# Kernel optimization log

Measured on AMD Instinct MI355X. Metric: run time of the kernel, lower is better.

## Reference

```python
import math
import jax, jax.numpy as jnp
import numpy as np

PHI = (1.0 + math.sqrt(5.0)) / 2.0
LUT_N = 4096
TWO_PI = 2.0 * math.pi


def _lut_tables():
    angles = jnp.arange(LUT_N, dtype=jnp.float32) * (TWO_PI / LUT_N)
    return jnp.sin(angles), jnp.cos(angles)


def _lut_sin_cos(theta, sin_t, cos_t):
    # quantize angle to nearest LUT entry, wrap mod 2*pi
    idx = jnp.mod(jnp.round(theta * (LUT_N / TWO_PI)).astype(jnp.int32), LUT_N)
    return jnp.take(sin_t, idx), jnp.take(cos_t, idx)


def setup_inputs() -> dict:
    key = jax.random.key(0)
    ks = jax.random.split(key, 8)
    B, D, H = 4096, 4096, 16
    Dh = D // H
    return {
        'x_real': jax.random.normal(ks[0], (B, D), dtype=jnp.float32),
        'x_imag': jax.random.normal(ks[1], (B, D), dtype=jnp.float32),
        't': jax.random.uniform(ks[2], (B,), dtype=jnp.float32) * 100.0,
        'trigger_real': jax.random.normal(ks[3], (H, Dh), dtype=jnp.float32) * 0.5,
        'trigger_imag': jax.random.normal(ks[4], (H, Dh), dtype=jnp.float32) * 0.5,
        'w_query': jax.random.normal(ks[5], (H, Dh), dtype=jnp.float32) * 0.02,
        'b_query': jnp.zeros((H, Dh), dtype=jnp.float32),
        'w_out': jax.random.normal(ks[6], (D,), dtype=jnp.float32) * 0.02,
        'b_out': jnp.zeros((D,), dtype=jnp.float32),
        'beta': jnp.abs(jax.random.normal(ks[7], (D,), dtype=jnp.float32)) * 5.0 + 5.0,
    }


def reference(x_real, x_imag, t, trigger_real, trigger_imag, w_query, b_query, w_out, b_out, beta):
    sin_t, cos_t = _lut_tables()
    B, D = x_real.shape
    H, Dh = trigger_real.shape

    # ---- per-head interference (vectorized over heads) ----
    xr = x_real.reshape(B, H, Dh)
    xi = x_imag.reshape(B, H, Dh)
    t_phi_h = (t * PHI)[:, None, None]                       # (B,1,1)
    wavelength_q = 1.0 + jnp.abs(w_query)                    # (H,Dh)
    theta_r = xr / wavelength_q + b_query + t_phi_h
    theta_i = xi / wavelength_q + b_query + t_phi_h
    sin_r, cos_r = _lut_sin_cos(theta_r, sin_t, cos_t)
    sin_i, cos_i = _lut_sin_cos(theta_i, sin_t, cos_t)
    q_real = cos_r * cos_i - sin_r * sin_i                   # (B,H,Dh)
    q_imag = cos_r * sin_i + sin_r * cos_i
    int_r = (q_real * trigger_real + q_imag * trigger_imag).sum(-1)   # (B,H)
    int_i = (q_real * trigger_imag - q_imag * trigger_real).sum(-1)
    total_int_real = int_r.mean(-1)                          # (B,)
    total_int_imag = int_i.mean(-1)

    # ---- constant-Q memory update (fresh memory = zeros) ----
    beta_eff = 1.0 / (1.0 + jnp.abs(beta))                   # (D,)
    w_eff = 1.0 / (1.0 + jnp.abs(w_out))                     # (D,)
    decay = jnp.minimum(jnp.exp(-beta_eff * w_eff), 0.9999)
    int_mag = jnp.sqrt(total_int_real ** 2 + total_int_imag ** 2 + 1e-8)[:, None]  # (B,1)
    write_scale = (w_eff * (1.0 - decay))[None, :]           # (1,D)
    # initial memory is zero -> memory*decay term vanishes
    mem_real = x_real * int_mag * write_scale
    mem_imag = x_imag * int_mag * write_scale

    # ---- Euler projection of memory ----
    wavelength = 1.0 + jnp.abs(w_out)
    t_phi = (t * PHI)[:, None]
    th_or = mem_real / wavelength + b_out + t_phi
    th_oi = mem_imag / wavelength + b_out + t_phi
    sin_or, cos_or = _lut_sin_cos(th_or, sin_t, cos_t)
    sin_oi, cos_oi = _lut_sin_cos(th_oi, sin_t, cos_t)
    out_real = cos_or * cos_oi - sin_or * sin_oi
    out_imag = cos_or * sin_oi + sin_or * cos_oi
    return out_real, out_imag
```

## Files before the change

### kernel.cpp

```cpp
#include <hip/hip_runtime.h>

#define LUT_N 4096
#define DVAL  4096
#define TPB   256

static constexpr double TWO_PI_D = 6.283185307179586476925286766559;
#define PHI_F 1.61803398874989484820f

__device__ __forceinline__ float fc(const float4& f, int j) {
    switch (j) { case 0: return f.x; case 1: return f.y; case 2: return f.z; }
    return f.w;
}
__device__ __forceinline__ void sc4(float4& f, int j, float v) {
    switch (j) { case 0: f.x = v; return; case 1: f.y = v; return; case 2: f.z = v; return; }
    f.w = v;
}
__device__ __forceinline__ void grid_sincos(float thr, float thi, float cidx,
                                            float& s_out, float& c_out) {
    float r = rintf(thr * cidx);
    float s = rintf(thi * cidx);
    float rev = (r + s) * (1.0f / (float)LUT_N);
    float frac = rev - floorf(rev);
    s_out = __builtin_amdgcn_sinf(frac);
    c_out = __builtin_amdgcn_cosf(frac);
}

__global__ __launch_bounds__(256) void echo_precompute(
    const float* __restrict__ w_query,
    const float* __restrict__ w_out,
    const float* __restrict__ beta,
    float* __restrict__ invq,
    float* __restrict__ wsi)
{
    int i = blockIdx.x * 256 + threadIdx.x;
    if (i < DVAL) {
        float inv_q     = 1.0f / (1.0f + fabsf(w_query[i]));
        float w_eff     = 1.0f / (1.0f + fabsf(w_out[i]));
        float beta_eff  = 1.0f / (1.0f + fabsf(beta[i]));
        float decay     = fminf(expf(-beta_eff * w_eff), 0.9999f);
        invq[i] = inv_q;
        wsi[i]  = (w_eff * (1.0f - decay)) * w_eff;
    }
}

template<bool USE_WS>
__global__ __launch_bounds__(TPB, 4) void echo_main(
    const float* __restrict__ x_real,
    const float* __restrict__ x_imag,
    const float* __restrict__ t,
    const float* __restrict__ trig_r,
    const float* __restrict__ trig_i,
    const float* __restrict__ w_query,
    const float* __restrict__ b_query,
    const float* __restrict__ w_out,
    const float* __restrict__ b_out,
    const float* __restrict__ beta,
    const float* __restrict__ invqG,
    const float* __restrict__ wsiG,
    float* __restrict__ out,
    int B)
{
    __shared__ float redR[4], redI[4];
    __shared__ float magS;

    const int tid = threadIdx.x;
    const int row = blockIdx.x;
    const float cidx = (float)((double)LUT_N / TWO_PI_D);

    const float tphi = t[row] * PHI_F;
    const float* xr = x_real + (size_t)row * DVAL;
    const float* xi = x_imag + (size_t)row * DVAL;

    float4 xr_s[4], xi_s[4];
    float accr = 0.0f, acci = 0.0f;

    #pragma unroll
    for (int k = 0; k < 4; ++k) {
        int v = tid + TPB * k;
        float4 a = ((const float4*)xr)[v];
        float4 c = ((const float4*)xi)[v];
        xr_s[k] = a; xi_s[k] = c;

        float4 iv4;
        if constexpr (USE_WS) {
            iv4 = ((const float4*)invqG)[v];
        } else {
            float4 wq4 = ((const float4*)w_query)[v];
            iv4 = make_float4(1.0f / (1.0f + fabsf(wq4.x)), 1.0f / (1.0f + fabsf(wq4.y)),
                              1.0f / (1.0f + fabsf(wq4.z)), 1.0f / (1.0f + fabsf(wq4.w)));
        }
        float4 bq4 = ((const float4*)b_query)[v];
        float4 tr4 = ((const float4*)trig_r)[v];
        float4 ti4 = ((const float4*)trig_i)[v];

        #pragma unroll
        for (int j = 0; j < 4; ++j) {
            float iv = fc(iv4, j), bq = fc(bq4, j);
            float thr = __builtin_fmaf(fc(a, j), iv, bq) + tphi;
            float thi = __builtin_fmaf(fc(c, j), iv, bq) + tphi;
            float q_i, q_r;
            grid_sincos(thr, thi, cidx, q_i, q_r);
            accr = __builtin_fmaf(q_r, fc(tr4, j), __builtin_fmaf(q_i, fc(ti4, j), accr));
            acci = __builtin_fmaf(q_r, fc(ti4, j), __builtin_fmaf(-q_i, fc(tr4, j), acci));
        }
    }

    #pragma unroll
    for (int m = 32; m >= 1; m >>= 1) {
        accr += __shfl_xor(accr, m, 64);
        acci += __shfl_xor(acci, m, 64);
    }
    if ((tid & 63) == 0) { redR[tid >> 6] = accr; redI[tid >> 6] = acci; }
    __syncthreads();
    if (tid == 0) {
        float tr = (redR[0] + redR[1] + redR[2] + redR[3]) * 0.0625f;
        float ti = (redI[0] + redI[1] + redI[2] + redI[3]) * 0.0625f;
        magS = sqrtf(tr * tr + ti * ti + 1e-8f);
    }
    __syncthreads();
    const float mag = magS;

    float4* outR = (float4*)(out + (size_t)row * DVAL);
    float4* outI = (float4*)(out + (size_t)B * DVAL + (size_t)row * DVAL);

    #pragma unroll
    for (int k = 0; k < 4; ++k) {
        int v = tid + TPB * k;
        float4 ws4;
        if constexpr (USE_WS) {
            ws4 = ((const float4*)wsiG)[v];
        } else {
            float4 wo4 = ((const float4*)w_out)[v];
            float4 be4 = ((const float4*)beta)[v];
            #pragma unroll
            for (int j = 0; j < 4; ++j) {
                float w_eff = 1.0f / (1.0f + fabsf(fc(wo4, j)));
                float beta_eff = 1.0f / (1.0f + fabsf(fc(be4, j)));
                float decay = fminf(expf(-beta_eff * w_eff), 0.9999f);
                sc4(ws4, j, (w_eff * (1.0f - decay)) * w_eff);
            }
        }
        float4 bo4 = ((const float4*)b_out)[v];

        float4 oR, oI;
        #pragma unroll
        for (int j = 0; j < 4; ++j) {
            float wsi_j = fc(ws4, j), bo = fc(bo4, j);
            float xmr = fc(xr_s[k], j) * mag;
            float xmi = fc(xi_s[k], j) * mag;
            float thr = __builtin_fmaf(xmr, wsi_j, bo) + tphi;
            float thi = __builtin_fmaf(xmi, wsi_j, bo) + tphi;
            float s_o, c_o;
            grid_sincos(thr, thi, cidx, s_o, c_o);
            sc4(oR, j, c_o);
            sc4(oI, j, s_o);
        }
        outR[v] = oR;
        outI[v] = oI;
    }
}

extern "C" void kernel_launch(void* const* d_in, const int* in_sizes, int n_in,
                              void* d_out, int out_size, void* d_ws, size_t ws_size,
                              hipStream_t stream) {
    const float* x_real    = (const float*)d_in[0];
    const float* x_imag    = (const float*)d_in[1];
    const float* t         = (const float*)d_in[2];
    const float* trig_r    = (const float*)d_in[3];
    const float* trig_i    = (const float*)d_in[4];
    const float* w_query   = (const float*)d_in[5];
    const float* b_query   = (const float*)d_in[6];
    const float* w_out     = (const float*)d_in[7];
    const float* b_out     = (const float*)d_in[8];
    const float* beta      = (const float*)d_in[9];
    float* out = (float*)d_out;

    const int B = in_sizes[2];
    const size_t need = 2 * (size_t)DVAL * sizeof(float);

    if (d_ws != nullptr && ws_size >= need) {
        float* invq = (float*)d_ws;
        float* wsi  = invq + DVAL;
        echo_precompute<<<DVAL / 256, 256, 0, stream>>>(w_query, w_out, beta, invq, wsi);
        echo_main<true><<<B, TPB, 0, stream>>>(
            x_real, x_imag, t, trig_r, trig_i, w_query, b_query, w_out, b_out, beta,
            invq, wsi, out, B);
    } else {
        echo_main<false><<<B, TPB, 0, stream>>>(
            x_real, x_imag, t, trig_r, trig_i, w_query, b_query, w_out, b_out, beta,
            nullptr, nullptr, out, B);
    }
}
```

Baseline: 261.8 us.

## Split fused row kernel into magnitude reduction and grid-stride projection kernels

Replaces the single per-row kernel with two launches: one computes the per-row interference magnitude into workspace, and a second grid-stride kernel does the Euler projection over all elements. This removes the in-block barrier between reduction and projection and decouples their occupancy. In exchange, x_real and x_imag are read from memory twice, and the workspace must now also hold B floats.

```diff
diff --git a/kernel.cpp b/kernel.cpp
--- a/kernel.cpp
+++ b/kernel.cpp
@@ -43,8 +43,117 @@
     }
 }
 
-template<bool USE_WS>
-__global__ __launch_bounds__(TPB, 4) void echo_main(
+__global__ __launch_bounds__(TPB) void echo_mag(
+    const float* __restrict__ x_real,
+    const float* __restrict__ x_imag,
+    const float* __restrict__ t,
+    const float* __restrict__ trig_r,
+    const float* __restrict__ trig_i,
+    const float* __restrict__ b_query,
+    const float* __restrict__ invqG,
+    float* __restrict__ magG)
+{
+    __shared__ float redR[4], redI[4];
+
+    const int tid = threadIdx.x;
+    const int row = blockIdx.x;
+    const float cidx = (float)((double)LUT_N / TWO_PI_D);
+
+    const float tphi = t[row] * PHI_F;
+    const float* xr = x_real + (size_t)row * DVAL;
+    const float* xi = x_imag + (size_t)row * DVAL;
+
+    float accr = 0.0f, acci = 0.0f;
+
+    #pragma unroll
+    for (int k = 0; k < 4; ++k) {
+        int v = tid + TPB * k;
+        float4 a   = ((const float4*)xr)[v];
+        float4 c   = ((const float4*)xi)[v];
+        float4 iv4 = ((const float4*)invqG)[v];
+        float4 bq4 = ((const float4*)b_query)[v];
+        float4 tr4 = ((const float4*)trig_r)[v];
+        float4 ti4 = ((const float4*)trig_i)[v];
+
+        #pragma unroll
+        for (int j = 0; j < 4; ++j) {
+            float iv = fc(iv4, j), bq = fc(bq4, j);
+            float thr = __builtin_fmaf(fc(a, j), iv, bq) + tphi;
+            float thi = __builtin_fmaf(fc(c, j), iv, bq) + tphi;
+            float q_i, q_r;
+            grid_sincos(thr, thi, cidx, q_i, q_r);
+            accr = __builtin_fmaf(q_r, fc(tr4, j), __builtin_fmaf(q_i, fc(ti4, j), accr));
+            acci = __builtin_fmaf(q_r, fc(ti4, j), __builtin_fmaf(-q_i, fc(tr4, j), acci));
+        }
+    }
+
+    #pragma unroll
+    for (int m = 32; m >= 1; m >>= 1) {
+        accr += __shfl_xor(accr, m, 64);
+        acci += __shfl_xor(acci, m, 64);
+    }
+    if ((tid & 63) == 0) { redR[tid >> 6] = accr; redI[tid >> 6] = acci; }
+    __syncthreads();
+    if (tid == 0) {
+        float tr = (redR[0] + redR[1] + redR[2] + redR[3]) * 0.0625f;
+        float ti = (redI[0] + redI[1] + redI[2] + redI[3]) * 0.0625f;
+        magG[row] = sqrtf(tr * tr + ti * ti + 1e-8f);
+    }
+}
+
+__global__ __launch_bounds__(TPB, 4) void echo_proj(
+    const float* __restrict__ x_real,
+    const float* __restrict__ x_imag,
+    const float* __restrict__ t,
+    const float* __restrict__ b_out,
+    const float* __restrict__ wsiG,
+    const float* __restrict__ magG,
+    float* __restrict__ out,
+    int B, int nblocks)
+{
+    const float cidx = (float)((double)LUT_N / TWO_PI_D);
+    const int nvec_row = DVAL / 4;
+    const long total   = (long)B * nvec_row;
+    const long stride  = (long)nblocks * TPB;
+    long g = (long)blockIdx.x * TPB + threadIdx.x;
+
+    const float4* xr4 = (const float4*)x_real;
+    const float4* xi4 = (const float4*)x_imag;
+    const float4* bo4G = (const float4*)b_out;
+    const float4* ws4G = (const float4*)wsiG;
+    float4* outR = (float4*)out;
+    float4* outI = (float4*)(out + (size_t)B * DVAL);
+
+    #pragma unroll 4
+    for (long i = g; i < total; i += stride) {
+        int row  = (int)(i >> 10);
+        int col4 = (int)(i & 1023);
+
+        float4 a   = xr4[i];
+        float4 c   = xi4[i];
+        float4 ws4 = ws4G[col4];
+        float4 bo  = bo4G[col4];
+        float mag  = magG[row];
+        float tphi = t[row] * PHI_F;
+
+        float4 oR, oI;
+        #pragma unroll
+        for (int j = 0; j < 4; ++j) {
+            float xmr = fc(a, j) * mag;
+            float xmi = fc(c, j) * mag;
+            float thr = __builtin_fmaf(xmr, fc(ws4, j), fc(bo, j)) + tphi;
+            float thi = __builtin_fmaf(xmi, fc(ws4, j), fc(bo, j)) + tphi;
+            float s_o, c_o;
+            grid_sincos(thr, thi, cidx, s_o, c_o);
+            sc4(oR, j, c_o);
+            sc4(oI, j, s_o);
+        }
+        outR[i] = oR;
+        outI[i] = oI;
+    }
+}
+
+__global__ __launch_bounds__(TPB, 4) void echo_single(
     const float* __restrict__ x_real,
     const float* __restrict__ x_imag,
     const float* __restrict__ t,
@@ -55,8 +164,6 @@
     const float* __restrict__ w_out,
     const float* __restrict__ b_out,
     const float* __restrict__ beta,
-    const float* __restrict__ invqG,
-    const float* __restrict__ wsiG,
     float* __restrict__ out,
     int B)
 {
@@ -80,19 +187,12 @@
         float4 a = ((const float4*)xr)[v];
         float4 c = ((const float4*)xi)[v];
         xr_s[k] = a; xi_s[k] = c;
-
-        float4 iv4;
-        if constexpr (USE_WS) {
-            iv4 = ((const float4*)invqG)[v];
-        } else {
-            float4 wq4 = ((const float4*)w_query)[v];
-            iv4 = make_float4(1.0f / (1.0f + fabsf(wq4.x)), 1.0f / (1.0f + fabsf(wq4.y)),
-                              1.0f / (1.0f + fabsf(wq4.z)), 1.0f / (1.0f + fabsf(wq4.w)));
-        }
+        float4 wq4 = ((const float4*)w_query)[v];
+        float4 iv4 = make_float4(1.0f / (1.0f + fabsf(wq4.x)), 1.0f / (1.0f + fabsf(wq4.y)),
+                                 1.0f / (1.0f + fabsf(wq4.z)), 1.0f / (1.0f + fabsf(wq4.w)));
         float4 bq4 = ((const float4*)b_query)[v];
         float4 tr4 = ((const float4*)trig_r)[v];
         float4 ti4 = ((const float4*)trig_i)[v];
-
         #pragma unroll
         for (int j = 0; j < 4; ++j) {
             float iv = fc(iv4, j), bq = fc(bq4, j);
@@ -104,7 +204,6 @@
             acci = __builtin_fmaf(q_r, fc(ti4, j), __builtin_fmaf(-q_i, fc(tr4, j), acci));
         }
     }
-
     #pragma unroll
     for (int m = 32; m >= 1; m >>= 1) {
         accr += __shfl_xor(accr, m, 64);
@@ -122,34 +221,27 @@
 
     float4* outR = (float4*)(out + (size_t)row * DVAL);
     float4* outI = (float4*)(out + (size_t)B * DVAL + (size_t)row * DVAL);
-
     #pragma unroll
     for (int k = 0; k < 4; ++k) {
         int v = tid + TPB * k;
+        float4 wo4 = ((const float4*)w_out)[v];
+        float4 be4 = ((const float4*)beta)[v];
         float4 ws4;
-        if constexpr (USE_WS) {
-            ws4 = ((const float4*)wsiG)[v];
-        } else {
-            float4 wo4 = ((const float4*)w_out)[v];
-            float4 be4 = ((const float4*)beta)[v];
-            #pragma unroll
-            for (int j = 0; j < 4; ++j) {
-                float w_eff = 1.0f / (1.0f + fabsf(fc(wo4, j)));
-                float beta_eff = 1.0f / (1.0f + fabsf(fc(be4, j)));
-                float decay = fminf(expf(-beta_eff * w_eff), 0.9999f);
-                sc4(ws4, j, (w_eff * (1.0f - decay)) * w_eff);
-            }
+        #pragma unroll
+        for (int j = 0; j < 4; ++j) {
+            float w_eff = 1.0f / (1.0f + fabsf(fc(wo4, j)));
+            float beta_eff = 1.0f / (1.0f + fabsf(fc(be4, j)));
+            float decay = fminf(expf(-beta_eff * w_eff), 0.9999f);
+            sc4(ws4, j, (w_eff * (1.0f - decay)) * w_eff);
         }
         float4 bo4 = ((const float4*)b_out)[v];
-
         float4 oR, oI;
         #pragma unroll
         for (int j = 0; j < 4; ++j) {
-            float wsi_j = fc(ws4, j), bo = fc(bo4, j);
             float xmr = fc(xr_s[k], j) * mag;
             float xmi = fc(xi_s[k], j) * mag;
-            float thr = __builtin_fmaf(xmr, wsi_j, bo) + tphi;
-            float thi = __builtin_fmaf(xmi, wsi_j, bo) + tphi;
+            float thr = __builtin_fmaf(xmr, fc(ws4, j), fc(bo4, j)) + tphi;
+            float thi = __builtin_fmaf(xmi, fc(ws4, j), fc(bo4, j)) + tphi;
             float s_o, c_o;
             grid_sincos(thr, thi, cidx, s_o, c_o);
             sc4(oR, j, c_o);
@@ -176,18 +268,21 @@
     float* out = (float*)d_out;
 
     const int B = in_sizes[2];
-    const size_t need = 2 * (size_t)DVAL * sizeof(float);
+    const size_t need = (2 * (size_t)DVAL + (size_t)B) * sizeof(float);
 
     if (d_ws != nullptr && ws_size >= need) {
         float* invq = (float*)d_ws;
         float* wsi  = invq + DVAL;
+        float* mag  = wsi + DVAL;
         echo_precompute<<<DVAL / 256, 256, 0, stream>>>(w_query, w_out, beta, invq, wsi);
-        echo_main<true><<<B, TPB, 0, stream>>>(
+        echo_mag<<<B, TPB, 0, stream>>>(x_real, x_imag, t, trig_r, trig_i, b_query,
+                                        invq, mag);
+        const int nblocks = 2048;
+        echo_proj<<<nblocks, TPB, 0, stream>>>(x_real, x_imag, t, b_out, wsi, mag,
+                                               out, B, nblocks);
+    } else {
+        echo_single<<<B, TPB, 0, stream>>>(
             x_real, x_imag, t, trig_r, trig_i, w_query, b_query, w_out, b_out, beta,
-            invq, wsi, out, B);
-    } else {
-        echo_main<false><<<B, TPB, 0, stream>>>(
-            x_real, x_imag, t, trig_r, trig_i, w_query, b_query, w_out, b_out, beta,
-            nullptr, nullptr, out, B);
-    }
-}
+            out, B);
+    }
+}
```

After: 276.7 us. 5.7% more time.

## Process four rows per block with register double-buffered prefetch of next row

Applied to the files above, without the earlier changes.

Each block now handles four consecutive rows instead of one. While it computes the current row, it loads the next row's x_real/x_imag into a second set of registers, so global memory latency overlaps with compute. This cuts the grid size by four and doubles the registers used for row data, which can lower occupancy under the launch bounds and reduce the number of blocks available to balance across CUs. Rows beyond B are clamped to B-1, which recomputes and rewrites the last row.

```diff
diff --git a/kernel.cpp b/kernel.cpp
--- a/kernel.cpp
+++ b/kernel.cpp
@@ -3,6 +3,7 @@
 #define LUT_N 4096
 #define DVAL  4096
 #define TPB   256
+#define RPB   4
 
 static constexpr double TWO_PI_D = 6.283185307179586476925286766559;
 #define PHI_F 1.61803398874989484820f
@@ -44,7 +45,7 @@
 }
 
 template<bool USE_WS>
-__global__ __launch_bounds__(TPB, 4) void echo_main(
+__global__ __launch_bounds__(TPB, 4) void echo_persist(
     const float* __restrict__ x_real,
     const float* __restrict__ x_imag,
     const float* __restrict__ t,
@@ -63,100 +64,128 @@
     __shared__ float redR[4], redI[4];
     __shared__ float magS;
 
-    const int tid = threadIdx.x;
-    const int row = blockIdx.x;
+    const int tid  = threadIdx.x;
+    const int row0 = blockIdx.x * RPB;
     const float cidx = (float)((double)LUT_N / TWO_PI_D);
 
-    const float tphi = t[row] * PHI_F;
-    const float* xr = x_real + (size_t)row * DVAL;
-    const float* xi = x_imag + (size_t)row * DVAL;
-
-    float4 xr_s[4], xi_s[4];
-    float accr = 0.0f, acci = 0.0f;
+    float4 curR[4], curI[4], nxtR[4], nxtI[4];
+
+    {
+        int row = min(row0, B - 1);
+        const float4* xr4 = (const float4*)(x_real + (size_t)row * DVAL);
+        const float4* xi4 = (const float4*)(x_imag + (size_t)row * DVAL);
+        #pragma unroll
+        for (int k = 0; k < 4; ++k) {
+            curR[k] = xr4[tid + TPB * k];
+            curI[k] = xi4[tid + TPB * k];
+        }
+    }
 
     #pragma unroll
-    for (int k = 0; k < 4; ++k) {
-        int v = tid + TPB * k;
-        float4 a = ((const float4*)xr)[v];
-        float4 c = ((const float4*)xi)[v];
-        xr_s[k] = a; xi_s[k] = c;
-
-        float4 iv4;
-        if constexpr (USE_WS) {
-            iv4 = ((const float4*)invqG)[v];
-        } else {
-            float4 wq4 = ((const float4*)w_query)[v];
-            iv4 = make_float4(1.0f / (1.0f + fabsf(wq4.x)), 1.0f / (1.0f + fabsf(wq4.y)),
-                              1.0f / (1.0f + fabsf(wq4.z)), 1.0f / (1.0f + fabsf(wq4.w)));
-        }
-        float4 bq4 = ((const float4*)b_query)[v];
-        float4 tr4 = ((const float4*)trig_r)[v];
-        float4 ti4 = ((const float4*)trig_i)[v];
-
-        #pragma unroll
-        for (int j = 0; j < 4; ++j) {
-            float iv = fc(iv4, j), bq = fc(bq4, j);
-            float thr = __builtin_fmaf(fc(a, j), iv, bq) + tphi;
-            float thi = __builtin_fmaf(fc(c, j), iv, bq) + tphi;
-            float q_i, q_r;
-            grid_sincos(thr, thi, cidx, q_i, q_r);
-            accr = __builtin_fmaf(q_r, fc(tr4, j), __builtin_fmaf(q_i, fc(ti4, j), accr));
-            acci = __builtin_fmaf(q_r, fc(ti4, j), __builtin_fmaf(-q_i, fc(tr4, j), acci));
-        }
-    }
-
-    #pragma unroll
-    for (int m = 32; m >= 1; m >>= 1) {
-        accr += __shfl_xor(accr, m, 64);
-        acci += __shfl_xor(acci, m, 64);
-    }
-    if ((tid & 63) == 0) { redR[tid >> 6] = accr; redI[tid >> 6] = acci; }
-    __syncthreads();
-    if (tid == 0) {
-        float tr = (redR[0] + redR[1] + redR[2] + redR[3]) * 0.0625f;
-        float ti = (redI[0] + redI[1] + redI[2] + redI[3]) * 0.0625f;
-        magS = sqrtf(tr * tr + ti * ti + 1e-8f);
-    }
-    __syncthreads();
-    const float mag = magS;
-
-    float4* outR = (float4*)(out + (size_t)row * DVAL);
-    float4* outI = (float4*)(out + (size_t)B * DVAL + (size_t)row * DVAL);
-
-    #pragma unroll
-    for (int k = 0; k < 4; ++k) {
-        int v = tid + TPB * k;
-        float4 ws4;
-        if constexpr (USE_WS) {
-            ws4 = ((const float4*)wsiG)[v];
-        } else {
-            float4 wo4 = ((const float4*)w_out)[v];
-            float4 be4 = ((const float4*)beta)[v];
+    for (int r = 0; r < RPB; ++r) {
+        const int row = min(row0 + r, B - 1);
+
+        if (r + 1 < RPB) {
+            int nrow = min(row0 + r + 1, B - 1);
+            const float4* xr4 = (const float4*)(x_real + (size_t)nrow * DVAL);
+            const float4* xi4 = (const float4*)(x_imag + (size_t)nrow * DVAL);
+            #pragma unroll
+            for (int k = 0; k < 4; ++k) {
+                nxtR[k] = xr4[tid + TPB * k];
+                nxtI[k] = xi4[tid + TPB * k];
+            }
+        }
+
+        const float tphi = t[row] * PHI_F;
+        float accr = 0.0f, acci = 0.0f;
+
+        #pragma unroll
+        for (int k = 0; k < 4; ++k) {
+            int v = tid + TPB * k;
+            float4 iv4;
+            if constexpr (USE_WS) {
+                iv4 = ((const float4*)invqG)[v];
+            } else {
+                float4 wq4 = ((const float4*)w_query)[v];
+                iv4 = make_float4(1.0f / (1.0f + fabsf(wq4.x)), 1.0f / (1.0f + fabsf(wq4.y)),
+                                  1.0f / (1.0f + fabsf(wq4.z)), 1.0f / (1.0f + fabsf(wq4.w)));
+            }
+            float4 bq4 = ((const float4*)b_query)[v];
+            float4 tr4 = ((const float4*)trig_r)[v];
+            float4 ti4 = ((const float4*)trig_i)[v];
+
             #pragma unroll
             for (int j = 0; j < 4; ++j) {
-                float w_eff = 1.0f / (1.0f + fabsf(fc(wo4, j)));
-                float beta_eff = 1.0f / (1.0f + fabsf(fc(be4, j)));
-                float decay = fminf(expf(-beta_eff * w_eff), 0.9999f);
-                sc4(ws4, j, (w_eff * (1.0f - decay)) * w_eff);
-            }
-        }
-        float4 bo4 = ((const float4*)b_out)[v];
-
-        float4 oR, oI;
-        #pragma unroll
-        for (int j = 0; j < 4; ++j) {
-            float wsi_j = fc(ws4, j), bo = fc(bo4, j);
-            float xmr = fc(xr_s[k], j) * mag;
-            float xmi = fc(xi_s[k], j) * mag;
-            float thr = __builtin_fmaf(xmr, wsi_j, bo) + tphi;
-            float thi = __builtin_fmaf(xmi, wsi_j, bo) + tphi;
-            float s_o, c_o;
-            grid_sincos(thr, thi, cidx, s_o, c_o);
-            sc4(oR, j, c_o);
-            sc4(oI, j, s_o);
-        }
-        outR[v] = oR;
-        outI[v] = oI;
+                float iv = fc(iv4, j), bq = fc(bq4, j);
+                float thr = __builtin_fmaf(fc(curR[k], j), iv, bq) + tphi;
+                float thi = __builtin_fmaf(fc(curI[k], j), iv, bq) + tphi;
+                float q_i, q_r;
+                grid_sincos(thr, thi, cidx, q_i, q_r);
+                accr = __builtin_fmaf(q_r, fc(tr4, j), __builtin_fmaf(q_i, fc(ti4, j), accr));
+                acci = __builtin_fmaf(q_r, fc(ti4, j), __builtin_fmaf(-q_i, fc(tr4, j), acci));
+            }
+        }
+
+        #pragma unroll
+        for (int m = 32; m >= 1; m >>= 1) {
+            accr += __shfl_xor(accr, m, 64);
+            acci += __shfl_xor(acci, m, 64);
+        }
+        if ((tid & 63) == 0) { redR[tid >> 6] = accr; redI[tid >> 6] = acci; }
+        __syncthreads();
+        if (tid == 0) {
+            float tr = (redR[0] + redR[1] + redR[2] + redR[3]) * 0.0625f;
+            float ti = (redI[0] + redI[1] + redI[2] + redI[3]) * 0.0625f;
+            magS = sqrtf(tr * tr + ti * ti + 1e-8f);
+        }
+        __syncthreads();
+        const float mag = magS;
+
+        float4* outR = (float4*)(out + (size_t)row * DVAL);
+        float4* outI = (float4*)(out + (size_t)B * DVAL + (size_t)row * DVAL);
+
+        #pragma unroll
+        for (int k = 0; k < 4; ++k) {
+            int v = tid + TPB * k;
+            float4 ws4;
+            if constexpr (USE_WS) {
+                ws4 = ((const float4*)wsiG)[v];
+            } else {
+                float4 wo4 = ((const float4*)w_out)[v];
+                float4 be4 = ((const float4*)beta)[v];
+                #pragma unroll
+                for (int j = 0; j < 4; ++j) {
+                    float w_eff = 1.0f / (1.0f + fabsf(fc(wo4, j)));
+                    float beta_eff = 1.0f / (1.0f + fabsf(fc(be4, j)));
+                    float decay = fminf(expf(-beta_eff * w_eff), 0.9999f);
+                    sc4(ws4, j, (w_eff * (1.0f - decay)) * w_eff);
+                }
+            }
+            float4 bo4 = ((const float4*)b_out)[v];
+
+            float4 oR, oI;
+            #pragma unroll
+            for (int j = 0; j < 4; ++j) {
+                float xmr = fc(curR[k], j) * mag;
+                float xmi = fc(curI[k], j) * mag;
+                float thr = __builtin_fmaf(xmr, fc(ws4, j), fc(bo4, j)) + tphi;
+                float thi = __builtin_fmaf(xmi, fc(ws4, j), fc(bo4, j)) + tphi;
+                float s_o, c_o;
+                grid_sincos(thr, thi, cidx, s_o, c_o);
+                sc4(oR, j, c_o);
+                sc4(oI, j, s_o);
+            }
+            outR[v] = oR;
+            outI[v] = oI;
+        }
+
+        if (r + 1 < RPB) {
+            #pragma unroll
+            for (int k = 0; k < 4; ++k) {
+                curR[k] = nxtR[k];
+                curI[k] = nxtI[k];
+            }
+        }
     }
 }
 
@@ -176,17 +205,18 @@
     float* out = (float*)d_out;
 
     const int B = in_sizes[2];
+    const int nblocks = (B + RPB - 1) / RPB;
     const size_t need = 2 * (size_t)DVAL * sizeof(float);
 
     if (d_ws != nullptr && ws_size >= need) {
         float* invq = (float*)d_ws;
         float* wsi  = invq + DVAL;
         echo_precompute<<<DVAL / 256, 256, 0, stream>>>(w_query, w_out, beta, invq, wsi);
-        echo_main<true><<<B, TPB, 0, stream>>>(
+        echo_persist<true><<<nblocks, TPB, 0, stream>>>(
             x_real, x_imag, t, trig_r, trig_i, w_query, b_query, w_out, b_out, beta,
             invq, wsi, out, B);
     } else {
-        echo_main<false><<<B, TPB, 0, stream>>>(
+        echo_persist<false><<<nblocks, TPB, 0, stream>>>(
             x_real, x_imag, t, trig_r, trig_i, w_query, b_query, w_out, b_out, beta,
             nullptr, nullptr, out, B);
     }
```

Result: no change. 263.6 us (+0.7%).
